# Kernel tuning notes

Measured on AMD Instinct MI355X. Metric: run time of the kernel, lower is better.

## Reference

```python
import jax, jax.numpy as jnp
import numpy as np

# --- configuration (from init_kwargs / chosen production scale) ---
NUM_STEPS = 18
SIGMA_MIN = 0.002
SIGMA_MAX = 80.0
RHO = 7.0
CE_SIGMA = 0.2
SIGMA_DATA = 0.5  # standard EDM preconditioning constant for the surrogate net
N_CES = 2
B, C, H, W = 64, 3, 64, 64
NUM_CLASSES = 1000


def _t_steps():
    # Karras sigma schedule, computed in float64 numpy then cast (original uses fp64).
    i = np.arange(NUM_STEPS, dtype=np.float64)
    ts = (SIGMA_MAX ** (1.0 / RHO) + i / (NUM_STEPS - 1) * (SIGMA_MIN ** (1.0 / RHO) - SIGMA_MAX ** (1.0 / RHO))) ** RHO
    ts = np.concatenate([ts, np.zeros(1)])  # append t_N = 0 (net.round_sigma ~ identity)
    return jnp.asarray(ts, dtype=jnp.float32)


def _net(x, sigma, W_net, b_net):
    # EDM-preconditioned denoiser surrogate: D(x) = c_skip*x + c_out*F(c_in*x)
    s2 = sigma * sigma
    denom = s2 + SIGMA_DATA ** 2
    c_skip = SIGMA_DATA ** 2 / denom
    c_out = sigma * SIGMA_DATA * jax.lax.rsqrt(denom)
    c_in = jax.lax.rsqrt(denom)
    f = jax.lax.conv_general_dilated(c_in * x, W_net, (1, 1), 'SAME',
                                     dimension_numbers=('NCHW', 'OIHW', 'NCHW'))
    f = f + b_net[None, :, None, None]
    return c_skip * x + c_out * f


def _sample(mu_ce, latents, noise, W_net, b_net):
    # EDM Euler ODE/SDE sampler with counterfactual drift toward mu_ce.
    ts = _t_steps()  # [NUM_STEPS+1]
    x0 = latents * ts[0]

    def step(x_cur, inp):
        t_cur, t_next, eps = inp
        denoised = _net(x_cur, t_cur, W_net, b_net)
        dx_dt = (denoised - x_cur) / t_cur + t_cur * (mu_ce - x_cur) / (CE_SIGMA ** 2 + t_cur * t_cur)
        # eps is pre-zeroed for the last two steps (i >= NUM_STEPS-2)
        x_next = x_cur + 2.0 * dx_dt * (t_cur - t_next) + jnp.sqrt(2.0 * t_cur * (t_cur - t_next)) * eps
        return x_next, None

    x_final, _ = jax.lax.scan(step, x0, (ts[:-1], ts[1:], noise))
    return x_final


def setup_inputs() -> dict:
    key = jax.random.key(0)
    k_x, k_lat, k_noise, k_wn, k_wc = jax.random.split(key, 5)
    x = jax.random.uniform(k_x, (B, C, H, W), dtype=jnp.float32)  # images in [0,1]
    latents = jax.random.normal(k_lat, (N_CES * B, C, H, W), dtype=jnp.float32)
    noise = jax.random.normal(k_noise, (NUM_STEPS, N_CES * B, C, H, W), dtype=jnp.float32)
    # noise is only injected for i < NUM_STEPS - 2
    mask = (jnp.arange(NUM_STEPS) < NUM_STEPS - 2).astype(jnp.float32)
    noise = noise * mask[:, None, None, None, None]
    W_net = 0.05 * jax.random.normal(k_wn, (C, C, 3, 3), dtype=jnp.float32)  # OIHW
    b_net = jnp.zeros((C,), dtype=jnp.float32)
    W_cls = 0.02 * jax.random.normal(k_wc, (C * H * W, NUM_CLASSES), dtype=jnp.float32)
    b_cls = jnp.zeros((NUM_CLASSES,), dtype=jnp.float32)
    return {"x": x, "latents": latents, "noise": noise,
            "W_net": W_net, "b_net": b_net, "W_cls": W_cls, "b_cls": b_cls}


def reference(x, latents, noise, W_net, b_net, W_cls, b_cls):
    xt = jnp.tile(x, (N_CES, 1, 1, 1))          # [n_ces*B, C, H, W]
    mu_ce = 2.0 * xt - 1.0                      # rescale to [-1, 1]
    x_ces = (_sample(mu_ce, latents, noise, W_net, b_net) + 1.0) / 2.0
    logits = x_ces.reshape(N_CES * B, -1) @ W_cls + b_cls  # cls surrogate
    logits = jax.nn.logsumexp(logits.reshape(N_CES, B, NUM_CLASSES), axis=0) - jnp.log(float(N_CES))
    return logits
```

## Files before the change

kernel.cpp:

```cpp
#include <hip/hip_runtime.h>
#include <math.h>

#define NSTEPS 18
#define NS 128
#define CHW 12288
#define HW 4096
#define NCLS 1000
#define WR 50

#define SWZ(off) ((off) ^ ((((off) >> 8) & 7) << 4))

struct StepC { float c_skip, c_out, c_in, inv_t, ce, two_dt, nc, pad; };
struct Steps { StepC s[NSTEPS]; float t0; };

typedef __attribute__((ext_vector_type(8))) short v8s;
typedef __attribute__((ext_vector_type(4))) float v4f;

__device__ __forceinline__ unsigned short f2bf(float f) {
    unsigned int u = __float_as_uint(f);
    unsigned int r = (u + 0x7FFFu + ((u >> 16) & 1u)) >> 16;
    return (unsigned short)r;
}

__global__ __launch_bounds__(448, 2)
void sampler_kernel(const float* __restrict__ x, const float* __restrict__ latents,
                    const float* __restrict__ noise, const float* __restrict__ Wn_g,
                    const float* __restrict__ bn_g, unsigned short* __restrict__ Aout, Steps S)
{
    __shared__ float xs[3 * WR * 64];
    __shared__ float Wn[81];
    __shared__ float bn[3];
    char* xb = (char*)xs;
    const int tid = threadIdx.x;
    const int n = blockIdx.x >> 1;
    const int q = blockIdx.x & 1;
    const int base = q << 5;
    const int w0 = (base - 18 > 0) ? base - 18 : 0;
    const int w1 = (base + 50 < 64) ? base + 50 : 64;
    const int wsize = w1 - w0;

    if (tid < 81) Wn[tid] = Wn_g[tid];
    if (tid < 3)  bn[tid] = bn_g[tid];

    const float t0 = S.t0;
    const float* lat = latents + (size_t)n * CHW;

    #pragma unroll
    for (int ci = 0; ci < 3; ++ci)
        for (int u = tid; u < wsize * 16; u += 448) {
            const int lr2 = u >> 4, c4 = (u & 15) << 2;
            float4 v = *reinterpret_cast<const float4*>(lat + ci * HW + (w0 + lr2) * 64 + c4);
            v.x *= t0; v.y *= t0; v.z *= t0; v.w *= t0;
            const int off = (ci * 3200 + lr2 * 64 + c4) << 2;
            *reinterpret_cast<float4*>(xb + SWZ(off)) = v;
        }

    const int lr = tid >> 3;
    const int sc = tid & 7;
    const int cbase = sc << 3;
    const int gr = w0 + lr;
    const bool rowv = (lr < wsize);
    __syncthreads();

    float xc[3][8];
    if (rowv) {
        #pragma unroll
        for (int ci = 0; ci < 3; ++ci) {
            const int bo = (ci * 3200 + lr * 64 + cbase) << 2;
            float4 a = *reinterpret_cast<const float4*>(xb + SWZ(bo));
            float4 b = *reinterpret_cast<const float4*>(xb + SWZ(bo + 16));
            xc[ci][0]=a.x; xc[ci][1]=a.y; xc[ci][2]=a.z; xc[ci][3]=a.w;
            xc[ci][4]=b.x; xc[ci][5]=b.y; xc[ci][6]=b.z; xc[ci][7]=b.w;
        }
    }

    const float* xin = x + (size_t)(n & 63) * CHW;
    float mu[3][8];
    if (rowv) {
        #pragma unroll
        for (int co = 0; co < 3; ++co) {
            const float* mb = xin + co * HW + gr * 64 + cbase;
            float4 m0 = *reinterpret_cast<const float4*>(mb);
            float4 m1 = *reinterpret_cast<const float4*>(mb + 4);
            mu[co][0] = 2.f*m0.x - 1.f; mu[co][1] = 2.f*m0.y - 1.f;
            mu[co][2] = 2.f*m0.z - 1.f; mu[co][3] = 2.f*m0.w - 1.f;
            mu[co][4] = 2.f*m1.x - 1.f; mu[co][5] = 2.f*m1.y - 1.f;
            mu[co][6] = 2.f*m1.z - 1.f; mu[co][7] = 2.f*m1.w - 1.f;
        }
    }

    for (int step = 0; step < NSTEPS; ++step) {
        const StepC c = S.s[step];
        const int lo = base - 17 + step;
        const int hi = base + 49 - step;
        const bool active = rowv && (gr >= lo) && (gr < hi);

        if (active) {
            float acc[3][8];
            #pragma unroll
            for (int co = 0; co < 3; ++co)
                #pragma unroll
                for (int j = 0; j < 8; ++j) acc[co][j] = 0.f;

            #pragma unroll
            for (int ci = 0; ci < 3; ++ci) {
                float in0[10], in2[10], cen[10];
                if (gr - 1 >= 0) {
                    const int bo = (ci * 3200 + (lr - 1) * 64 + cbase) << 2;
                    float4 a = *reinterpret_cast<const float4*>(xb + SWZ(bo));
                    float4 b = *reinterpret_cast<const float4*>(xb + SWZ(bo + 16));
                    in0[1]=a.x; in0[2]=a.y; in0[3]=a.z; in0[4]=a.w;
                    in0[5]=b.x; in0[6]=b.y; in0[7]=b.z; in0[8]=b.w;
                    in0[0] = (sc > 0) ? __shfl_up(in0[8], 1) : 0.f;
                    in0[9] = (sc < 7) ? __shfl_down(in0[1], 1) : 0.f;
                } else {
                    #pragma unroll
                    for (int p = 0; p < 10; ++p) in0[p] = 0.f;
                }
                if (gr + 1 < 64) {
                    const int bo = (ci * 3200 + (lr + 1) * 64 + cbase) << 2;
                    float4 a = *reinterpret_cast<const float4*>(xb + SWZ(bo));
                    float4 b = *reinterpret_cast<const float4*>(xb + SWZ(bo + 16));
                    in2[1]=a.x; in2[2]=a.y; in2[3]=a.z; in2[4]=a.w;
                    in2[5]=b.x; in2[6]=b.y; in2[7]=b.z; in2[8]=b.w;
                    in2[0] = (sc > 0) ? __shfl_up(in2[8], 1) : 0.f;
                    in2[9] = (sc < 7) ? __shfl_down(in2[1], 1) : 0.f;
                } else {
                    #pragma unroll
                    for (int p = 0; p < 10; ++p) in2[p] = 0.f;
                }
                cen[0] = (sc > 0) ? __shfl_up(xc[ci][7], 1) : 0.f;
                cen[9] = (sc < 7) ? __shfl_down(xc[ci][0], 1) : 0.f;
                #pragma unroll
                for (int j = 0; j < 8; ++j) cen[j + 1] = xc[ci][j];

                #pragma unroll
                for (int co = 0; co < 3; ++co) {
                    const int wb = (co * 3 + ci) * 9;
                    #pragma unroll
                    for (int dw = 0; dw < 3; ++dw) {
                        const float w0t = Wn[wb + dw];
                        const float w1t = Wn[wb + 3 + dw];
                        const float w2t = Wn[wb + 6 + dw];
                        #pragma unroll
                        for (int j = 0; j < 8; ++j) {
                            acc[co][j] = fmaf(w0t, in0[j + dw], acc[co][j]);
                            acc[co][j] = fmaf(w1t, cen[j + dw], acc[co][j]);
                            acc[co][j] = fmaf(w2t, in2[j + dw], acc[co][j]);
                        }
                    }
                }
            }

            const float* nz = noise + ((size_t)(step * NS + n)) * CHW;
            #pragma unroll
            for (int co = 0; co < 3; ++co) {
                float eps[8];
                if (step < NSTEPS - 2) {
                    const float* nb = nz + co * HW + gr * 64 + cbase;
                    float4 e0 = *reinterpret_cast<const float4*>(nb);
                    float4 e1 = *reinterpret_cast<const float4*>(nb + 4);
                    eps[0]=e0.x; eps[1]=e0.y; eps[2]=e0.z; eps[3]=e0.w;
                    eps[4]=e1.x; eps[5]=e1.y; eps[6]=e1.z; eps[7]=e1.w;
                } else {
                    #pragma unroll
                    for (int j = 0; j < 8; ++j) eps[j] = 0.f;
                }
                #pragma unroll
                for (int j = 0; j < 8; ++j) {
                    const float xv = xc[co][j];
                    const float f = fmaf(c.c_in, acc[co][j], bn[co]);
                    const float den = c.c_skip * xv + c.c_out * f;
                    const float dx = (den - xv) * c.inv_t + c.ce * (mu[co][j] - xv);
                    xc[co][j] = fmaf(c.two_dt, dx, fmaf(c.nc, eps[j], xv));
                }
            }
        }
        __syncthreads();
        if (active) {
            #pragma unroll
            for (int co = 0; co < 3; ++co) {
                const int wo = (co * 3200 + lr * 64 + cbase) << 2;
                *reinterpret_cast<float4*>(xb + SWZ(wo)) =
                    make_float4(xc[co][0], xc[co][1], xc[co][2], xc[co][3]);
                *reinterpret_cast<float4*>(xb + SWZ(wo + 16)) =
                    make_float4(xc[co][4], xc[co][5], xc[co][6], xc[co][7]);
            }
        }
        __syncthreads();
    }

    unsigned short* Ao = Aout + (size_t)n * CHW;
    for (int u = tid; u < 3 * 32 * 16; u += 448) {
        const int ci = u >> 9;
        const int rem = u & 511;
        const int r = rem >> 4, c4 = (rem & 15) << 2;
        const int lrow = base + r - w0;
        const int off = (ci * 3200 + lrow * 64 + c4) << 2;
        float4 v = *reinterpret_cast<const float4*>(xb + SWZ(off));
        ushort4 o;
        o.x = f2bf((v.x + 1.f) * 0.5f); o.y = f2bf((v.y + 1.f) * 0.5f);
        o.z = f2bf((v.z + 1.f) * 0.5f); o.w = f2bf((v.w + 1.f) * 0.5f);
        *reinterpret_cast<ushort4*>(Ao + ci * HW + (base + r) * 64 + c4) = o;
    }
}

__global__ __launch_bounds__(256)
void gemm_kernel(const unsigned short* __restrict__ Abf, const float* __restrict__ Wc,
                 float* __restrict__ part, int bkc)
{
    const int tid = threadIdx.x;
    const int wv = tid >> 6;
    const int lane = tid & 63;
    const int lrow = lane & 15;
    const int lk8 = (lane >> 4) << 3;
    const int ct = blockIdx.x & 15;
    const int kc = blockIdx.x >> 4;
    const int c0 = ct << 6;
    const int k0 = kc * bkc;

    v4f acc[2][4];
    #pragma unroll
    for (int rt = 0; rt < 2; ++rt)
        #pragma unroll
        for (int c4 = 0; c4 < 4; ++c4) acc[rt][c4] = (v4f)0.f;

    #pragma unroll 2
    for (int kk = 0; kk < bkc; kk += 32) {
        const int kb = k0 + kk + lk8;
        v8s a[2];
        #pragma unroll
        for (int rt = 0; rt < 2; ++rt)
            a[rt] = *reinterpret_cast<const v8s*>(Abf + (size_t)(wv * 32 + rt * 16 + lrow) * CHW + kb);
        v8s b[4];
        #pragma unroll
        for (int c4 = 0; c4 < 4; ++c4) {
            const int col = c0 + c4 * 16 + lrow;
            const bool cv = (col < NCLS);
            #pragma unroll
            for (int j = 0; j < 8; ++j) {
                const float f = cv ? Wc[(size_t)(kb + j) * NCLS + col] : 0.f;
                b[c4][j] = (short)f2bf(f);
            }
        }
        #pragma unroll
        for (int rt = 0; rt < 2; ++rt)
            #pragma unroll
            for (int c4 = 0; c4 < 4; ++c4)
                acc[rt][c4] = __builtin_amdgcn_mfma_f32_16x16x32_bf16(a[rt], b[c4], acc[rt][c4], 0, 0, 0);
    }

    float* pp = part + (size_t)kc * NS * NCLS;
    #pragma unroll
    for (int rt = 0; rt < 2; ++rt)
        #pragma unroll
        for (int c4 = 0; c4 < 4; ++c4) {
            const int col = c0 + c4 * 16 + lrow;
            if (col < NCLS) {
                #pragma unroll
                for (int r = 0; r < 4; ++r) {
                    const int row = wv * 32 + rt * 16 + (lane >> 4) * 4 + r;
                    pp[(size_t)row * NCLS + col] = acc[rt][c4][r];
                }
            }
        }
}

__global__ __launch_bounds__(256)
void lse_kernel(const float* __restrict__ part, const float* __restrict__ bcls,
                float* __restrict__ out, int ks)
{
    const int i = blockIdx.x * 256 + threadIdx.x;
    if (i >= 64 * NCLS) return;
    const int b = i / NCLS;
    const int k = i - b * NCLS;
    float l0 = bcls[k], l1 = bcls[k];
    for (int kc = 0; kc < ks; ++kc) {
        l0 += part[(size_t)kc * NS * NCLS + (size_t)b * NCLS + k];
        l1 += part[(size_t)kc * NS * NCLS + (size_t)(b + 64) * NCLS + k];
    }
    const float m = fmaxf(l0, l1);
    out[i] = m + logf(expf(l0 - m) + expf(l1 - m)) - 0.69314718055994530942f;
}

extern "C" void kernel_launch(void* const* d_in, const int* in_sizes, int n_in,
                              void* d_out, int out_size, void* d_ws, size_t ws_size,
                              hipStream_t stream) {
    const float* x       = (const float*)d_in[0];
    const float* latents = (const float*)d_in[1];
    const float* noise   = (const float*)d_in[2];
    const float* W_net   = (const float*)d_in[3];
    const float* b_net   = (const float*)d_in[4];
    const float* W_cls   = (const float*)d_in[5];
    const float* b_cls   = (const float*)d_in[6];
    float* out = (float*)d_out;

    unsigned short* Amat = (unsigned short*)d_ws;
    const size_t amat_bytes = (size_t)NS * CHW * 2;
    float* part = (float*)((char*)d_ws + amat_bytes);

    Steps S;
    const double smin = pow(0.002, 1.0 / 7.0), smax = pow(80.0, 1.0 / 7.0);
    float tsf[NSTEPS + 1];
    for (int i = 0; i < NSTEPS; ++i) {
        double v = smax + (double)i / (double)(NSTEPS - 1) * (smin - smax);
        tsf[i] = (float)pow(v, 7.0);
    }
    tsf[NSTEPS] = 0.f;
    S.t0 = tsf[0];
    for (int i = 0; i < NSTEPS; ++i) {
        const float t = tsf[i], tn = tsf[i + 1];
        const float s2 = t * t, denom = s2 + 0.25f;
        StepC c;
        c.c_skip = 0.25f / denom;
        c.c_out  = t * 0.5f / sqrtf(denom);
        c.c_in   = 1.0f / sqrtf(denom);
        c.inv_t  = 1.0f / t;
        c.ce     = t / (0.04f + s2);
        const float dt = t - tn;
        c.two_dt = 2.f * dt;
        c.nc     = sqrtf(2.f * t * dt);
        c.pad    = 0.f;
        S.s[i] = c;
    }

    int KS = 32;
    while (KS > 1 && amat_bytes + (size_t)KS * NS * NCLS * 4 > ws_size) KS >>= 1;
    const int bkc = CHW / KS;

    sampler_kernel<<<NS * 2, 448, 0, stream>>>(x, latents, noise, W_net, b_net, Amat, S);
    gemm_kernel<<<16 * KS, 256, 0, stream>>>(Amat, W_cls, part, bkc);
    lse_kernel<<<(64 * NCLS + 255) / 256, 256, 0, stream>>>(part, b_cls, out, KS);
}
```

Before: 110.4 us.

## Double-buffer sampler halo tile and halve per-thread work to 4 columns

```diff
diff --git a/kernel.cpp b/kernel.cpp
--- a/kernel.cpp
+++ b/kernel.cpp
@@ -6,9 +6,8 @@
 #define CHW 12288
 #define HW 4096
 #define NCLS 1000
-#define WR 50
-
-#define SWZ(off) ((off) ^ ((((off) >> 8) & 7) << 4))
+#define WROWS 50
+#define BUFF (3 * WROWS * 64)
 
 struct StepC { float c_skip, c_out, c_in, inv_t, ce, two_dt, nc, pad; };
 struct Steps { StepC s[NSTEPS]; float t0; };
@@ -22,73 +21,49 @@
     return (unsigned short)r;
 }
 
-__global__ __launch_bounds__(448, 2)
+__global__ __launch_bounds__(832)
 void sampler_kernel(const float* __restrict__ x, const float* __restrict__ latents,
                     const float* __restrict__ noise, const float* __restrict__ Wn_g,
                     const float* __restrict__ bn_g, unsigned short* __restrict__ Aout, Steps S)
 {
-    __shared__ float xs[3 * WR * 64];
+    __shared__ float xs[2 * BUFF];
     __shared__ float Wn[81];
     __shared__ float bn[3];
-    char* xb = (char*)xs;
     const int tid = threadIdx.x;
     const int n = blockIdx.x >> 1;
     const int q = blockIdx.x & 1;
     const int base = q << 5;
-    const int w0 = (base - 18 > 0) ? base - 18 : 0;
-    const int w1 = (base + 50 < 64) ? base + 50 : 64;
-    const int wsize = w1 - w0;
+    const int w0 = q ? 14 : 0;
 
     if (tid < 81) Wn[tid] = Wn_g[tid];
     if (tid < 3)  bn[tid] = bn_g[tid];
 
+    const int lr = tid >> 4;
+    const int cg = tid & 15;
+    const int col = cg << 2;
+    const int gr = w0 + lr;
+    const bool rowv = (lr < WROWS);
+
     const float t0 = S.t0;
     const float* lat = latents + (size_t)n * CHW;
-
-    #pragma unroll
-    for (int ci = 0; ci < 3; ++ci)
-        for (int u = tid; u < wsize * 16; u += 448) {
-            const int lr2 = u >> 4, c4 = (u & 15) << 2;
-            float4 v = *reinterpret_cast<const float4*>(lat + ci * HW + (w0 + lr2) * 64 + c4);
+    const float* xin = x + (size_t)(n & 63) * CHW;
+
+    float xc[3][4], mu[3][4];
+    if (rowv) {
+        #pragma unroll
+        for (int ci = 0; ci < 3; ++ci) {
+            float4 v = *reinterpret_cast<const float4*>(lat + ci * HW + gr * 64 + col);
             v.x *= t0; v.y *= t0; v.z *= t0; v.w *= t0;
-            const int off = (ci * 3200 + lr2 * 64 + c4) << 2;
-            *reinterpret_cast<float4*>(xb + SWZ(off)) = v;
-        }
-
-    const int lr = tid >> 3;
-    const int sc = tid & 7;
-    const int cbase = sc << 3;
-    const int gr = w0 + lr;
-    const bool rowv = (lr < wsize);
+            xc[ci][0]=v.x; xc[ci][1]=v.y; xc[ci][2]=v.z; xc[ci][3]=v.w;
+            *reinterpret_cast<float4*>(&xs[(ci * WROWS + lr) * 64 + col]) = v;
+            float4 m = *reinterpret_cast<const float4*>(xin + ci * HW + gr * 64 + col);
+            mu[ci][0] = 2.f*m.x - 1.f; mu[ci][1] = 2.f*m.y - 1.f;
+            mu[ci][2] = 2.f*m.z - 1.f; mu[ci][3] = 2.f*m.w - 1.f;
+        }
+    }
     __syncthreads();
 
-    float xc[3][8];
-    if (rowv) {
-        #pragma unroll
-        for (int ci = 0; ci < 3; ++ci) {
-            const int bo = (ci * 3200 + lr * 64 + cbase) << 2;
-            float4 a = *reinterpret_cast<const float4*>(xb + SWZ(bo));
-            float4 b = *reinterpret_cast<const float4*>(xb + SWZ(bo + 16));
-            xc[ci][0]=a.x; xc[ci][1]=a.y; xc[ci][2]=a.z; xc[ci][3]=a.w;
-            xc[ci][4]=b.x; xc[ci][5]=b.y; xc[ci][6]=b.z; xc[ci][7]=b.w;
-        }
-    }
-
-    const float* xin = x + (size_t)(n & 63) * CHW;
-    float mu[3][8];
-    if (rowv) {
-        #pragma unroll
-        for (int co = 0; co < 3; ++co) {
-            const float* mb = xin + co * HW + gr * 64 + cbase;
-            float4 m0 = *reinterpret_cast<const float4*>(mb);
-            float4 m1 = *reinterpret_cast<const float4*>(mb + 4);
-            mu[co][0] = 2.f*m0.x - 1.f; mu[co][1] = 2.f*m0.y - 1.f;
-            mu[co][2] = 2.f*m0.z - 1.f; mu[co][3] = 2.f*m0.w - 1.f;
-            mu[co][4] = 2.f*m1.x - 1.f; mu[co][5] = 2.f*m1.y - 1.f;
-            mu[co][6] = 2.f*m1.z - 1.f; mu[co][7] = 2.f*m1.w - 1.f;
-        }
-    }
-
+    int cur = 0;
     for (int step = 0; step < NSTEPS; ++step) {
         const StepC c = S.s[step];
         const int lo = base - 17 + step;
@@ -96,43 +71,39 @@
         const bool active = rowv && (gr >= lo) && (gr < hi);
 
         if (active) {
-            float acc[3][8];
+            float acc[3][4];
             #pragma unroll
             for (int co = 0; co < 3; ++co)
                 #pragma unroll
-                for (int j = 0; j < 8; ++j) acc[co][j] = 0.f;
+                for (int j = 0; j < 4; ++j) acc[co][j] = 0.f;
 
             #pragma unroll
             for (int ci = 0; ci < 3; ++ci) {
-                float in0[10], in2[10], cen[10];
-                if (gr - 1 >= 0) {
-                    const int bo = (ci * 3200 + (lr - 1) * 64 + cbase) << 2;
-                    float4 a = *reinterpret_cast<const float4*>(xb + SWZ(bo));
-                    float4 b = *reinterpret_cast<const float4*>(xb + SWZ(bo + 16));
+                float in0[6], in2[6], cen[6];
+                if (gr >= 1) {
+                    float4 a = *reinterpret_cast<const float4*>(
+                        &xs[cur * BUFF + (ci * WROWS + lr - 1) * 64 + col]);
                     in0[1]=a.x; in0[2]=a.y; in0[3]=a.z; in0[4]=a.w;
-                    in0[5]=b.x; in0[6]=b.y; in0[7]=b.z; in0[8]=b.w;
-                    in0[0] = (sc > 0) ? __shfl_up(in0[8], 1) : 0.f;
-                    in0[9] = (sc < 7) ? __shfl_down(in0[1], 1) : 0.f;
+                    in0[0] = (cg > 0)  ? __shfl_up(a.w, 1)  : 0.f;
+                    in0[5] = (cg < 15) ? __shfl_down(a.x, 1) : 0.f;
                 } else {
                     #pragma unroll
-                    for (int p = 0; p < 10; ++p) in0[p] = 0.f;
+                    for (int p = 0; p < 6; ++p) in0[p] = 0.f;
                 }
                 if (gr + 1 < 64) {
-                    const int bo = (ci * 3200 + (lr + 1) * 64 + cbase) << 2;
-                    float4 a = *reinterpret_cast<const float4*>(xb + SWZ(bo));
-                    float4 b = *reinterpret_cast<const float4*>(xb + SWZ(bo + 16));
+                    float4 a = *reinterpret_cast<const float4*>(
+                        &xs[cur * BUFF + (ci * WROWS + lr + 1) * 64 + col]);
                     in2[1]=a.x; in2[2]=a.y; in2[3]=a.z; in2[4]=a.w;
-                    in2[5]=b.x; in2[6]=b.y; in2[7]=b.z; in2[8]=b.w;
-                    in2[0] = (sc > 0) ? __shfl_up(in2[8], 1) : 0.f;
-                    in2[9] = (sc < 7) ? __shfl_down(in2[1], 1) : 0.f;
+                    in2[0] = (cg > 0)  ? __shfl_up(a.w, 1)  : 0.f;
+                    in2[5] = (cg < 15) ? __shfl_down(a.x, 1) : 0.f;
                 } else {
                     #pragma unroll
-                    for (int p = 0; p < 10; ++p) in2[p] = 0.f;
-                }
-                cen[0] = (sc > 0) ? __shfl_up(xc[ci][7], 1) : 0.f;
-                cen[9] = (sc < 7) ? __shfl_down(xc[ci][0], 1) : 0.f;
-                #pragma unroll
-                for (int j = 0; j < 8; ++j) cen[j + 1] = xc[ci][j];
+                    for (int p = 0; p < 6; ++p) in2[p] = 0.f;
+                }
+                cen[0] = (cg > 0)  ? __shfl_up(xc[ci][3], 1)  : 0.f;
+                cen[5] = (cg < 15) ? __shfl_down(xc[ci][0], 1) : 0.f;
+                #pragma unroll
+                for (int j = 0; j < 4; ++j) cen[j + 1] = xc[ci][j];
 
                 #pragma unroll
                 for (int co = 0; co < 3; ++co) {
@@ -143,10 +114,10 @@
                         const float w1t = Wn[wb + 3 + dw];
                         const float w2t = Wn[wb + 6 + dw];
                         #pragma unroll
-                        for (int j = 0; j < 8; ++j) {
-                            acc[co][j] = fmaf(w0t, in0[j + dw], acc[co][j]);
-                            acc[co][j] = fmaf(w1t, cen[j + dw], acc[co][j]);
-                            acc[co][j] = fmaf(w2t, in2[j + dw], acc[co][j]);
+                        for (int j = 0; j < 4; ++j) {
+                            acc[co][j] = fmaf(w0t, in0[j + dw],
+                                         fmaf(w1t, cen[j + dw],
+                                         fmaf(w2t, in2[j + dw], acc[co][j])));
                         }
                     }
                 }
@@ -155,19 +126,13 @@
             const float* nz = noise + ((size_t)(step * NS + n)) * CHW;
             #pragma unroll
             for (int co = 0; co < 3; ++co) {
-                float eps[8];
+                float eps[4] = {0.f, 0.f, 0.f, 0.f};
                 if (step < NSTEPS - 2) {
-                    const float* nb = nz + co * HW + gr * 64 + cbase;
-                    float4 e0 = *reinterpret_cast<const float4*>(nb);
-                    float4 e1 = *reinterpret_cast<const float4*>(nb + 4);
-                    eps[0]=e0.x; eps[1]=e0.y; eps[2]=e0.z; eps[3]=e0.w;
-                    eps[4]=e1.x; eps[5]=e1.y; eps[6]=e1.z; eps[7]=e1.w;
-                } else {
-                    #pragma unroll
-                    for (int j = 0; j < 8; ++j) eps[j] = 0.f;
-                }
-                #pragma unroll
-                for (int j = 0; j < 8; ++j) {
+                    float4 e = *reinterpret_cast<const float4*>(nz + co * HW + gr * 64 + col);
+                    eps[0]=e.x; eps[1]=e.y; eps[2]=e.z; eps[3]=e.w;
+                }
+                #pragma unroll
+                for (int j = 0; j < 4; ++j) {
                     const float xv = xc[co][j];
                     const float f = fmaf(c.c_in, acc[co][j], bn[co]);
                     const float den = c.c_skip * xv + c.c_out * f;
@@ -175,33 +140,24 @@
                     xc[co][j] = fmaf(c.two_dt, dx, fmaf(c.nc, eps[j], xv));
                 }
             }
+            #pragma unroll
+            for (int co = 0; co < 3; ++co)
+                *reinterpret_cast<float4*>(&xs[(cur ^ 1) * BUFF + (co * WROWS + lr) * 64 + col]) =
+                    make_float4(xc[co][0], xc[co][1], xc[co][2], xc[co][3]);
         }
         __syncthreads();
-        if (active) {
-            #pragma unroll
-            for (int co = 0; co < 3; ++co) {
-                const int wo = (co * 3200 + lr * 64 + cbase) << 2;
-                *reinterpret_cast<float4*>(xb + SWZ(wo)) =
-                    make_float4(xc[co][0], xc[co][1], xc[co][2], xc[co][3]);
-                *reinterpret_cast<float4*>(xb + SWZ(wo + 16)) =
-                    make_float4(xc[co][4], xc[co][5], xc[co][6], xc[co][7]);
-            }
-        }
-        __syncthreads();
-    }
-
-    unsigned short* Ao = Aout + (size_t)n * CHW;
-    for (int u = tid; u < 3 * 32 * 16; u += 448) {
-        const int ci = u >> 9;
-        const int rem = u & 511;
-        const int r = rem >> 4, c4 = (rem & 15) << 2;
-        const int lrow = base + r - w0;
-        const int off = (ci * 3200 + lrow * 64 + c4) << 2;
-        float4 v = *reinterpret_cast<const float4*>(xb + SWZ(off));
-        ushort4 o;
-        o.x = f2bf((v.x + 1.f) * 0.5f); o.y = f2bf((v.y + 1.f) * 0.5f);
-        o.z = f2bf((v.z + 1.f) * 0.5f); o.w = f2bf((v.w + 1.f) * 0.5f);
-        *reinterpret_cast<ushort4*>(Ao + ci * HW + (base + r) * 64 + c4) = o;
+        cur ^= 1;
+    }
+
+    if (rowv && gr >= base && gr < base + 32) {
+        unsigned short* Ao = Aout + (size_t)n * CHW;
+        #pragma unroll
+        for (int ci = 0; ci < 3; ++ci) {
+            ushort4 o;
+            o.x = f2bf((xc[ci][0] + 1.f) * 0.5f); o.y = f2bf((xc[ci][1] + 1.f) * 0.5f);
+            o.z = f2bf((xc[ci][2] + 1.f) * 0.5f); o.w = f2bf((xc[ci][3] + 1.f) * 0.5f);
+            *reinterpret_cast<ushort4*>(Ao + ci * HW + gr * 64 + col) = o;
+        }
     }
 }
 
@@ -328,7 +284,7 @@
     while (KS > 1 && amat_bytes + (size_t)KS * NS * NCLS * 4 > ws_size) KS >>= 1;
     const int bkc = CHW / KS;
 
-    sampler_kernel<<<NS * 2, 448, 0, stream>>>(x, latents, noise, W_net, b_net, Amat, S);
+    sampler_kernel<<<NS * 2, 832, 0, stream>>>(x, latents, noise, W_net, b_net, Amat, S);
     gemm_kernel<<<16 * KS, 256, 0, stream>>>(Amat, W_cls, part, bkc);
     lse_kernel<<<(64 * NCLS + 255) / 256, 256, 0, stream>>>(part, b_cls, out, KS);
 }
```

After: 208.8 us. 1.89x slower.
